# Kernel tuning notes

Hardware: AMD Instinct MI355X
Metric: run time of the kernel (lower is better)

The kernel has to match this reference:

```python
import jax, jax.numpy as jnp
import numpy as np

L = 128  # side_len
B = 16   # batch of poses


def setup_inputs() -> dict:
    key = jax.random.key(0)
    k1, k2 = jax.random.split(key)
    rotmat = jax.random.normal(k1, (B, 3, 3), dtype=jnp.float32)
    vol = jax.random.normal(k2, (L, L, L), dtype=jnp.float32) * 0.1
    # buffer 'coords_<scale>': meshgrid of linspace(-1,1,L), stacked as [y,x,z]
    lin = jnp.linspace(-1.0, 1.0, L, dtype=jnp.float32)
    X, Y, Z = jnp.meshgrid(lin, lin, lin, indexing='ij')
    coords = jnp.stack([Y, X, Z], axis=-1).reshape(-1, 3)  # [L^3, 3]
    return {"rotmat": rotmat, "vol": vol, "coords": coords, "proj_axis": 3}


def _grid_sample_3d(vol, pts):
    """torch grid_sample (trilinear, align_corners=True, zeros padding).
    vol: [L,L,L] laid out (D,H,W); pts: [B,N,3] with last dim (x,y,z) in [-1,1],
    x indexing W (last vol dim), y indexing H, z indexing D."""
    Ld = vol.shape[0]
    idx = (pts + 1.0) * 0.5 * (Ld - 1)  # align_corners=True mapping
    x, y, z = idx[..., 0], idx[..., 1], idx[..., 2]
    x0 = jnp.floor(x); y0 = jnp.floor(y); z0 = jnp.floor(z)
    wx1 = x - x0; wy1 = y - y0; wz1 = z - z0
    wx0 = 1.0 - wx1; wy0 = 1.0 - wy1; wz0 = 1.0 - wz1
    x0i = x0.astype(jnp.int32); y0i = y0.astype(jnp.int32); z0i = z0.astype(jnp.int32)
    x1i = x0i + 1; y1i = y0i + 1; z1i = z0i + 1

    def gather(zi, yi, xi):
        valid = ((xi >= 0) & (xi < Ld) & (yi >= 0) & (yi < Ld)
                 & (zi >= 0) & (zi < Ld))
        v = vol[jnp.clip(zi, 0, Ld - 1), jnp.clip(yi, 0, Ld - 1),
                jnp.clip(xi, 0, Ld - 1)]
        return jnp.where(valid, v, 0.0)

    return (gather(z0i, y0i, x0i) * wz0 * wy0 * wx0
            + gather(z0i, y0i, x1i) * wz0 * wy0 * wx1
            + gather(z0i, y1i, x0i) * wz0 * wy1 * wx0
            + gather(z0i, y1i, x1i) * wz0 * wy1 * wx1
            + gather(z1i, y0i, x0i) * wz1 * wy0 * wx0
            + gather(z1i, y0i, x1i) * wz1 * wy0 * wx1
            + gather(z1i, y1i, x0i) * wz1 * wy1 * wx0
            + gather(z1i, y1i, x1i) * wz1 * wy1 * wx1)


def reference(rotmat, vol, coords, proj_axis):
    # pytorch3d Rotate.transform_points: row vectors -> points @ R
    pts = jnp.einsum('nj,bjk->bnk', coords, rotmat)       # [B, L^3, 3]
    rot_vol = _grid_sample_3d(vol, pts)                    # [B, L^3]
    Ld = vol.shape[-1]
    proj = rot_vol.reshape(-1, Ld, Ld, Ld).sum(axis=proj_axis)  # [B, L, L]
    return proj[:, None, :, :]                             # [B, 1, L, L]
```

## Files before the change

kernel.cpp:

```cpp
#include <hip/hip_runtime.h>
#include <hip/hip_fp16.h>

#define LSIDE 128
#define NB 16
#define PACKED_BYTES (LSIDE * LSIDE * LSIDE * 16)

union P8 { __half h[8]; int4 v; };

__global__ __launch_bounds__(256) void pack8_kernel(
    const float* __restrict__ vol, int4* __restrict__ packed)
{
    const int t = blockIdx.x * 256 + threadIdx.x;
    const int x = t & 127;
    const int y = (t >> 7) & 127;
    const int z = t >> 14;
    const int xp = min(x + 1, 127);
    const int yp = min(y + 1, 127);
    const int zp = min(z + 1, 127);
    const float* p00 = vol + (z  * LSIDE + y ) * LSIDE;
    const float* p01 = vol + (z  * LSIDE + yp) * LSIDE;
    const float* p10 = vol + (zp * LSIDE + y ) * LSIDE;
    const float* p11 = vol + (zp * LSIDE + yp) * LSIDE;
    P8 o;
    o.h[0] = __float2half(p00[x]); o.h[1] = __float2half(p00[xp]);
    o.h[2] = __float2half(p01[x]); o.h[3] = __float2half(p01[xp]);
    o.h[4] = __float2half(p10[x]); o.h[5] = __float2half(p10[xp]);
    o.h[6] = __float2half(p11[x]); o.h[7] = __float2half(p11[xp]);
    packed[t] = o.v;
}

__device__ __forceinline__ void clip1(float r, float c, float A, float B,
                                      float& lo, float& hi)
{
    if (fabsf(r) > 1e-12f) {
        const float inv = 1.0f / r;
        const float a = (A - c) * inv, e = (B - c) * inv;
        lo = fmaxf(lo, fminf(a, e));
        hi = fminf(hi, fmaxf(a, e));
    } else if (c < A || c > B) {
        lo = 1e9f; hi = -1e9f;
    }
}

#define BOUNDARY_RUN(ks, ke)                                                            \
    if ((ks) < (ke)) {                                                                  \
        float gx = fmaf(fmaf((float)(ks), h, -1.0f), r20, bx) * 63.5f + 63.5f;          \
        float gy = fmaf(fmaf((float)(ks), h, -1.0f), r21, by) * 63.5f + 63.5f;          \
        float gz = fmaf(fmaf((float)(ks), h, -1.0f), r22, bz) * 63.5f + 63.5f;          \
        for (int k = (ks); k < (ke); ++k) {                                             \
            const float fx = floorf(gx), fy = floorf(gy), fz = floorf(gz);              \
            const int x0 = (int)fx, y0 = (int)fy, z0 = (int)fz;                         \
            const float wx1 = gx - fx, wy1 = gy - fy, wz1 = gz - fz;                    \
            const float wx0m = ((unsigned)x0       < LSIDE) ? (1.0f - wx1) : 0.0f;      \
            const float wx1m = ((unsigned)(x0 + 1) < LSIDE) ? wx1 : 0.0f;               \
            const float wy0m = ((unsigned)y0       < LSIDE) ? (1.0f - wy1) : 0.0f;      \
            const float wy1m = ((unsigned)(y0 + 1) < LSIDE) ? wy1 : 0.0f;               \
            const float wz0m = ((unsigned)z0       < LSIDE) ? (1.0f - wz1) : 0.0f;      \
            const float wz1m = ((unsigned)(z0 + 1) < LSIDE) ? wz1 : 0.0f;               \
            const int cx0 = min(max(x0, 0), LSIDE - 1);                                 \
            const int cx1 = min(max(x0 + 1, 0), LSIDE - 1);                             \
            const int cy0 = min(max(y0, 0), LSIDE - 1) * LSIDE;                         \
            const int cy1 = min(max(y0 + 1, 0), LSIDE - 1) * LSIDE;                     \
            const int cz0 = min(max(z0, 0), LSIDE - 1) * LSIDE * LSIDE;                 \
            const int cz1 = min(max(z0 + 1, 0), LSIDE - 1) * LSIDE * LSIDE;             \
            const float v000 = vol[cz0 + cy0 + cx0];                                    \
            const float v001 = vol[cz0 + cy0 + cx1];                                    \
            const float v010 = vol[cz0 + cy1 + cx0];                                    \
            const float v011 = vol[cz0 + cy1 + cx1];                                    \
            const float v100 = vol[cz1 + cy0 + cx0];                                    \
            const float v101 = vol[cz1 + cy0 + cx1];                                    \
            const float v110 = vol[cz1 + cy1 + cx0];                                    \
            const float v111 = vol[cz1 + cy1 + cx1];                                    \
            gx += dxg; gy += dyg; gz += dzg;                                            \
            const float vx00 = v000 * wx0m + v001 * wx1m;                               \
            const float vx01 = v010 * wx0m + v011 * wx1m;                               \
            const float vx10 = v100 * wx0m + v101 * wx1m;                               \
            const float vx11 = v110 * wx0m + v111 * wx1m;                               \
            acc += (vx00 * wy0m + vx01 * wy1m) * wz0m                                   \
                 + (vx10 * wy0m + vx11 * wy1m) * wz1m;                                  \
        }                                                                               \
    }

#define INTERIOR_RUN(ks, ke)                                                            \
    if ((ks) < (ke)) {                                                                  \
        float gx = fmaf(fmaf((float)(ks), h, -1.0f), r20, bx) * 63.5f + 63.5f;          \
        float gy = fmaf(fmaf((float)(ks), h, -1.0f), r21, by) * 63.5f + 63.5f;          \
        float gz = fmaf(fmaf((float)(ks), h, -1.0f), r22, bz) * 63.5f + 63.5f;          \
        _Pragma("unroll 2")                                                             \
        for (int k = (ks); k < (ke); ++k) {                                             \
            const float fx = floorf(gx), fy = floorf(gy), fz = floorf(gz);              \
            const int x0 = (int)fx, y0 = (int)fy, z0 = (int)fz;                         \
            const float wx1 = gx - fx, wy1 = gy - fy, wz1 = gz - fz;                    \
            const float wx0 = 1.0f - wx1, wy0 = 1.0f - wy1, wz0 = 1.0f - wz1;           \
            P8 c;                                                                       \
            c.v = packed[(z0 * LSIDE + y0) * LSIDE + x0];                               \
            gx += dxg; gy += dyg; gz += dzg;                                            \
            const float v000 = __half2float(c.h[0]);                                    \
            const float v001 = __half2float(c.h[1]);                                    \
            const float v010 = __half2float(c.h[2]);                                    \
            const float v011 = __half2float(c.h[3]);                                    \
            const float v100 = __half2float(c.h[4]);                                    \
            const float v101 = __half2float(c.h[5]);                                    \
            const float v110 = __half2float(c.h[6]);                                    \
            const float v111 = __half2float(c.h[7]);                                    \
            const float p0 = (v000 * wx0 + v001 * wx1) * wy0                            \
                           + (v010 * wx0 + v011 * wx1) * wy1;                           \
            const float p1 = (v100 * wx0 + v101 * wx1) * wy0                            \
                           + (v110 * wx0 + v111 * wx1) * wy1;                           \
            acc += p0 * wz0 + p1 * wz1;                                                 \
        }                                                                               \
    }

__global__ __launch_bounds__(256) void ProjectorMultiRes_59236188947236_kernel(
    const float* __restrict__ rotmat,
    const float* __restrict__ vol,
    const int4* __restrict__ packed,
    const float* __restrict__ coords,
    float* __restrict__ out)
{
    __shared__ float lin[LSIDE];
    __shared__ float red[LSIDE];
    const int tid = threadIdx.x;
    if (tid < LSIDE) lin[tid] = coords[3 * tid + 2];
    __syncthreads();

    const int logical = (blockIdx.x & 7) * 256 + (blockIdx.x >> 3);
    const int b = logical >> 7;
    const int i = logical & 127;
    const int j = tid & 127;
    const int half = tid >> 7;

    const float* R = rotmat + b * 9;
    const float r00 = R[0], r01 = R[1], r02 = R[2];
    const float r10 = R[3], r11 = R[4], r12 = R[5];
    const float r20 = R[6], r21 = R[7], r22 = R[8];

    const float lj = lin[j];
    const float li = lin[i];
    const float bx = lj * r00 + li * r10;
    const float by = lj * r01 + li * r11;
    const float bz = lj * r02 + li * r12;

    const float h = 2.0f / 127.0f;

    const float Bd = 1.0f + 1.0f / 63.5f + 1e-4f;
    float lo = -1.0f, hi = 1.0f;
    clip1(r20, bx, -Bd, Bd, lo, hi);
    clip1(r21, by, -Bd, Bd, lo, hi);
    clip1(r22, bz, -Bd, Bd, lo, hi);
    int k0 = max((int)ceilf((lo + 1.0f) / h) - 1, 0);
    int k1 = min((int)floorf((hi + 1.0f) / h) + 2, LSIDE);
    if (k1 < k0) k1 = k0;

    const float AIN = 0.02f / 63.5f - 1.0f;
    const float BIN = 126.98f / 63.5f - 1.0f;
    float loi = -1.0f, hii = 1.0f;
    clip1(r20, bx, AIN, BIN, loi, hii);
    clip1(r21, by, AIN, BIN, loi, hii);
    clip1(r22, bz, AIN, BIN, loi, hii);
    int ia = (int)ceilf((loi + 1.0f) / h) + 1;
    int ib = (int)floorf((hii + 1.0f) / h);
    ia = min(max(ia, k0), k1);
    ib = min(max(ib, ia), k1);

    const float dxg = h * r20 * 63.5f;
    const float dyg = h * r21 * 63.5f;
    const float dzg = h * r22 * 63.5f;

    const int cnt  = k1 - k0;
    const int kmid = k0 + ((cnt + 1) >> 1);
    const int ks = half ? kmid : k0;
    const int ke = half ? k1   : kmid;

    const int s1e = min(ke, max(ks, ia));
    const int s2s = min(max(ks, ia), ke);
    const int s2e = min(max(ks, ib), ke);
    const int s3s = min(ke, max(ks, ib));

    float acc = 0.0f;
    BOUNDARY_RUN(ks, s1e)
    INTERIOR_RUN(s2s, s2e)
    BOUNDARY_RUN(s3s, ke)

    if (half) red[j] = acc;
    __syncthreads();
    if (!half) out[(b * LSIDE + i) * LSIDE + j] = acc + red[j];
}

extern "C" void kernel_launch(void* const* d_in, const int* in_sizes, int n_in,
                              void* d_out, int out_size, void* d_ws, size_t ws_size,
                              hipStream_t stream) {
    const float* rotmat = (const float*)d_in[0];
    const float* vol    = (const float*)d_in[1];
    const float* coords = (const float*)d_in[2];
    float* out = (float*)d_out;

    int4* packed = (int4*)d_ws;
    pack8_kernel<<<(LSIDE * LSIDE * LSIDE) / 256, 256, 0, stream>>>(vol, packed);
    ProjectorMultiRes_59236188947236_kernel<<<NB * LSIDE, 256, 0, stream>>>(
        rotmat, vol, packed, coords, out);
}
```

Before: 96.25 us.

## Split ray march into four segments per output and batch four gathers per iteration

```diff
diff --git a/kernel.cpp b/kernel.cpp
--- a/kernel.cpp
+++ b/kernel.cpp
@@ -3,7 +3,6 @@
 
 #define LSIDE 128
 #define NB 16
-#define PACKED_BYTES (LSIDE * LSIDE * LSIDE * 16)
 
 union P8 { __half h[8]; int4 v; };
 
@@ -40,6 +39,30 @@
     } else if (c < A || c > B) {
         lo = 1e9f; hi = -1e9f;
     }
+}
+
+__device__ __forceinline__ void cellw(float gx, float gy, float gz,
+                                      int& idx, float& wx, float& wy, float& wz)
+{
+    const float fx = floorf(gx), fy = floorf(gy), fz = floorf(gz);
+    idx = ((int)fz * LSIDE + (int)fy) * LSIDE + (int)fx;
+    wx = gx - fx; wy = gy - fy; wz = gz - fz;
+}
+
+__device__ __forceinline__ float trilerp8(int4 cv, float wx1, float wy1, float wz1)
+{
+    P8 c; c.v = cv;
+    const float wx0 = 1.0f - wx1, wy0 = 1.0f - wy1, wz0 = 1.0f - wz1;
+    const float v000 = __half2float(c.h[0]);
+    const float v001 = __half2float(c.h[1]);
+    const float v010 = __half2float(c.h[2]);
+    const float v011 = __half2float(c.h[3]);
+    const float v100 = __half2float(c.h[4]);
+    const float v101 = __half2float(c.h[5]);
+    const float v110 = __half2float(c.h[6]);
+    const float v111 = __half2float(c.h[7]);
+    return ((v000 * wx0 + v001 * wx1) * wy0 + (v010 * wx0 + v011 * wx1) * wy1) * wz0
+         + ((v100 * wx0 + v101 * wx1) * wy0 + (v110 * wx0 + v111 * wx1) * wy1) * wz1;
 }
 
 #define BOUNDARY_RUN(ks, ke)                                                            \
@@ -86,28 +109,30 @@
         float gx = fmaf(fmaf((float)(ks), h, -1.0f), r20, bx) * 63.5f + 63.5f;          \
         float gy = fmaf(fmaf((float)(ks), h, -1.0f), r21, by) * 63.5f + 63.5f;          \
         float gz = fmaf(fmaf((float)(ks), h, -1.0f), r22, bz) * 63.5f + 63.5f;          \
-        _Pragma("unroll 2")                                                             \
-        for (int k = (ks); k < (ke); ++k) {                                             \
-            const float fx = floorf(gx), fy = floorf(gy), fz = floorf(gz);              \
-            const int x0 = (int)fx, y0 = (int)fy, z0 = (int)fz;                         \
-            const float wx1 = gx - fx, wy1 = gy - fy, wz1 = gz - fz;                    \
-            const float wx0 = 1.0f - wx1, wy0 = 1.0f - wy1, wz0 = 1.0f - wz1;           \
-            P8 c;                                                                       \
-            c.v = packed[(z0 * LSIDE + y0) * LSIDE + x0];                               \
+        int k = (ks);                                                                   \
+        for (; k + 4 <= (ke); k += 4) {                                                 \
+            int i0, i1, i2, i3;                                                         \
+            float xa, ya, za, xb, yb, zb, xc, yc, zc, xd, yd, zd;                       \
+            cellw(gx,              gy,              gz,              i0, xa, ya, za);   \
+            cellw(gx +        dxg, gy +        dyg, gz +        dzg, i1, xb, yb, zb);   \
+            cellw(gx + 2.0f * dxg, gy + 2.0f * dyg, gz + 2.0f * dzg, i2, xc, yc, zc);   \
+            cellw(gx + 3.0f * dxg, gy + 3.0f * dyg, gz + 3.0f * dzg, i3, xd, yd, zd);   \
+            const int4 c0 = packed[i0];                                                 \
+            const int4 c1 = packed[i1];                                                 \
+            const int4 c2 = packed[i2];                                                 \
+            const int4 c3 = packed[i3];                                                 \
+            gx += 4.0f * dxg; gy += 4.0f * dyg; gz += 4.0f * dzg;                       \
+            acc  += trilerp8(c0, xa, ya, za);                                           \
+            acc2 += trilerp8(c1, xb, yb, zb);                                           \
+            acc  += trilerp8(c2, xc, yc, zc);                                           \
+            acc2 += trilerp8(c3, xd, yd, zd);                                           \
+        }                                                                               \
+        for (; k < (ke); ++k) {                                                         \
+            int i0; float xa, ya, za;                                                   \
+            cellw(gx, gy, gz, i0, xa, ya, za);                                          \
+            const int4 c0 = packed[i0];                                                 \
             gx += dxg; gy += dyg; gz += dzg;                                            \
-            const float v000 = __half2float(c.h[0]);                                    \
-            const float v001 = __half2float(c.h[1]);                                    \
-            const float v010 = __half2float(c.h[2]);                                    \
-            const float v011 = __half2float(c.h[3]);                                    \
-            const float v100 = __half2float(c.h[4]);                                    \
-            const float v101 = __half2float(c.h[5]);                                    \
-            const float v110 = __half2float(c.h[6]);                                    \
-            const float v111 = __half2float(c.h[7]);                                    \
-            const float p0 = (v000 * wx0 + v001 * wx1) * wy0                            \
-                           + (v010 * wx0 + v011 * wx1) * wy1;                           \
-            const float p1 = (v100 * wx0 + v101 * wx1) * wy0                            \
-                           + (v110 * wx0 + v111 * wx1) * wy1;                           \
-            acc += p0 * wz0 + p1 * wz1;                                                 \
+            acc += trilerp8(c0, xa, ya, za);                                            \
         }                                                                               \
     }
 
@@ -119,16 +144,19 @@
     float* __restrict__ out)
 {
     __shared__ float lin[LSIDE];
-    __shared__ float red[LSIDE];
+    __shared__ float red[3][64];
     const int tid = threadIdx.x;
     if (tid < LSIDE) lin[tid] = coords[3 * tid + 2];
     __syncthreads();
 
-    const int logical = (blockIdx.x & 7) * 256 + (blockIdx.x >> 3);
-    const int b = logical >> 7;
-    const int i = logical & 127;
-    const int j = tid & 127;
-    const int half = tid >> 7;
+    const int logical = (blockIdx.x & 7) * 512 + (blockIdx.x >> 3);
+    const int b   = logical >> 8;
+    const int rem = logical & 255;
+    const int i   = rem >> 1;
+    const int jh  = rem & 1;
+    const int jl  = tid & 63;
+    const int j   = jh * 64 + jl;
+    const int q   = tid >> 6;
 
     const float* R = rotmat + b * 9;
     const float r00 = R[0], r01 = R[1], r02 = R[2];
@@ -167,24 +195,26 @@
     const float dyg = h * r21 * 63.5f;
     const float dzg = h * r22 * 63.5f;
 
-    const int cnt  = k1 - k0;
-    const int kmid = k0 + ((cnt + 1) >> 1);
-    const int ks = half ? kmid : k0;
-    const int ke = half ? k1   : kmid;
+    const int cnt = k1 - k0;
+    const int ks = k0 + ((cnt * q) >> 2);
+    const int ke = k0 + ((cnt * (q + 1)) >> 2);
 
     const int s1e = min(ke, max(ks, ia));
     const int s2s = min(max(ks, ia), ke);
     const int s2e = min(max(ks, ib), ke);
     const int s3s = min(ke, max(ks, ib));
 
-    float acc = 0.0f;
+    float acc = 0.0f, acc2 = 0.0f;
     BOUNDARY_RUN(ks, s1e)
     INTERIOR_RUN(s2s, s2e)
     BOUNDARY_RUN(s3s, ke)
-
-    if (half) red[j] = acc;
+    acc += acc2;
+
+    if (q) red[q - 1][jl] = acc;
     __syncthreads();
-    if (!half) out[(b * LSIDE + i) * LSIDE + j] = acc + red[j];
+    if (q == 0)
+        out[(b * LSIDE + i) * LSIDE + j] =
+            acc + red[0][jl] + red[1][jl] + red[2][jl];
 }
 
 extern "C" void kernel_launch(void* const* d_in, const int* in_sizes, int n_in,
@@ -197,6 +227,6 @@
 
     int4* packed = (int4*)d_ws;
     pack8_kernel<<<(LSIDE * LSIDE * LSIDE) / 256, 256, 0, stream>>>(vol, packed);
-    ProjectorMultiRes_59236188947236_kernel<<<NB * LSIDE, 256, 0, stream>>>(
+    ProjectorMultiRes_59236188947236_kernel<<<NB * LSIDE * 2, 256, 0, stream>>>(
         rotmat, vol, packed, coords, out);
 }
```

New measurement: 108.9 us. 13.1% more time.
